# Kernel optimization log

Measured on AMD Instinct MI355X. Metric: run time of the kernel, lower is better.

Reference implementation:

```python
import jax, jax.numpy as jnp
import numpy as np

LAYERS = [2, 1024, 512, 256, 128, 1]
LB = jnp.array([0.0, 0.0], dtype=jnp.float32)
UB = jnp.array([2.0 * np.pi, 1.0], dtype=jnp.float32)


def _block_diag_mask(num_blocks, bs1, bs2):
    return jnp.kron(jnp.eye(num_blocks, dtype=jnp.float32), jnp.ones((bs1, bs2), jnp.float32))


def _masks():
    # masks for l in range(2, num_Layers - 2) with num_Layers = len(LAYERS) = 6 -> l in {2, 3}
    width = [LAYERS[0]] + [(2 ** (i - 1)) * LAYERS[i] for i in range(1, len(LAYERS) - 1)] + [LAYERS[-1]]
    masks = []
    for l in range(2, len(LAYERS) - 2):
        num_blocks = 2 ** (l - 1)
        bs1 = width[l] // num_blocks
        bs2 = 2 * LAYERS[l + 1]
        masks.append(_block_diag_mask(num_blocks, bs1, bs2))
    return masks


def setup_inputs() -> dict:
    key = jax.random.key(0)
    ks = jax.random.split(key, 8)
    N = 65536
    H = 1024

    def xavier(k, fi, fo):
        lim = float(np.sqrt(6.0 / (fi + fo)))
        return jax.random.uniform(k, (fi, fo), jnp.float32, -lim, lim)

    X = jax.random.uniform(ks[0], (N, 2), jnp.float32, 0.0, 1.0) * (UB - LB) + LB
    return {
        "X": X,
        "W0": xavier(ks[1], 2, H), "b0": jnp.zeros((1, H), jnp.float32),
        "W1": xavier(ks[2], H, H), "b1": jnp.zeros((1, H), jnp.float32),
        "W2": xavier(ks[3], H, H), "b2": jnp.zeros((1, H), jnp.float32),
        "W3": xavier(ks[4], H, H), "b3": jnp.zeros((1, H), jnp.float32),
        "W_last": xavier(ks[5], H, 1), "b_last": jnp.zeros((1, 1), jnp.float32),
    }


def reference(X, W0, b0, W1, b1, W2, b2, W3, b3, W_last, b_last):
    mask2, mask3 = _masks()
    # input normalization to [-1, 1]
    h = 2.0 * (X - LB) / (UB - LB) - 1.0
    h = jnp.tanh(h @ W0 + b0)                 # layer 0: dense
    h = jnp.tanh(h @ W1 + b1)                 # layer 1: dense (no mask in forward)
    h = jnp.tanh(h @ (W2 * mask2) + b2)       # layer 2: block-diagonal masked
    h = jnp.tanh(h @ (W3 * mask3) + b3)       # layer 3: block-diagonal masked
    return h @ W_last + b_last                # output layer, [N, 1]
```

## Files before the change

### kernel.cpp

```cpp
#include <hip/hip_runtime.h>
#include <cstdint>
#include <cstddef>


typedef _Float16  f16x8   __attribute__((ext_vector_type(8)));
typedef float     floatx4 __attribute__((ext_vector_type(4)));
typedef float     floatx8 __attribute__((ext_vector_type(8)));

__device__ __forceinline__ float tanh_fast(float x) {
    float e = __expf(2.0f * x);
    return 1.0f - 2.0f / (e + 1.0f);
}

__global__ __launch_bounds__(256)
void transposeH(const float* __restrict__ W, _Float16* __restrict__ Wt) {
    __shared__ float tile[32][33];
    const int tx = threadIdx.x & 31;
    const int ty = threadIdx.x >> 5;
    #pragma unroll
    for (int j = 0; j < 4; ++j) {
        int r = ty + j * 8;
        tile[r][tx] = W[(size_t)(blockIdx.y * 32 + r) * 1024 + blockIdx.x * 32 + tx];
    }
    __syncthreads();
    #pragma unroll
    for (int j = 0; j < 4; ++j) {
        int r = ty + j * 8;
        Wt[(size_t)(blockIdx.x * 32 + r) * 1024 + blockIdx.y * 32 + tx] =
            (_Float16)tile[tx][r];
    }
}

__global__ __launch_bounds__(256)
void init_out(float* __restrict__ out, const float* __restrict__ bl) {
    out[blockIdx.x * 256 + threadIdx.x] = bl[0];
}

__global__ __launch_bounds__(256)
void layer0_kernel(const float* __restrict__ X, const float* __restrict__ W0,
                   const float* __restrict__ b0, _Float16* __restrict__ H) {
    const int idx = blockIdx.x * 256 + threadIdx.x;
    const int row = idx >> 7;
    const int j0  = (idx & 127) << 3;
    const float x0 = X[row * 2 + 0];
    const float x1 = X[row * 2 + 1];
    const float xa = x0 * 0.31830988618379067f - 1.0f;
    const float xb = 2.0f * x1 - 1.0f;
    floatx8 wa = *(const floatx8*)(W0 + j0);
    floatx8 wb = *(const floatx8*)(W0 + 1024 + j0);
    floatx8 bb = *(const floatx8*)(b0 + j0);
    f16x8 o;
    #pragma unroll
    for (int j = 0; j < 8; ++j) {
        float v = fmaf(xa, wa[j], fmaf(xb, wb[j], bb[j]));
        o[j] = (_Float16)tanh_fast(v);
    }
    *(f16x8*)(H + (size_t)row * 1024 + j0) = o;
}

template <bool FUSE>
__global__ __launch_bounds__(512)
void gemm_tanh_f16(const _Float16* __restrict__ A, const _Float16* __restrict__ Bt,
                   const float* __restrict__ bias, _Float16* __restrict__ C,
                   const float* __restrict__ Wl, float* __restrict__ out, int KB) {
    __shared__ _Float16 As[256 * 32];
    __shared__ _Float16 Bs[128 * 32];

    const int tid  = threadIdx.x;
    const int lane = tid & 63;
    const int wave = tid >> 6;
    const int m0 = blockIdx.x * 256;
    const int n0 = blockIdx.y * 128;
    const int kbeg   = (n0 / KB) * KB;
    const int kiters = KB >> 5;
    const int wm = (wave & 3) << 6;
    const int wn = (wave >> 2) << 6;
    const int r = lane & 15;
    const int q = lane >> 4;

    const int rowA0 = tid >> 2;
    const int rowA1 = 128 + rowA0;
    const int seg   = (tid & 3) << 3;
    const size_t gA0 = (size_t)(m0 + rowA0) * 1024 + kbeg + seg;
    const size_t gA1 = (size_t)(m0 + rowA1) * 1024 + kbeg + seg;
    const size_t gB  = (size_t)(n0 + rowA0) * 1024 + kbeg + seg;
    const int ldsA0 = tid * 8;
    const int ldsA1 = (512 + tid) * 8;
    const int ldsB  = tid * 8;

    floatx4 acc[4][4];
    #pragma unroll
    for (int i = 0; i < 4; ++i)
        #pragma unroll
        for (int j = 0; j < 4; ++j)
            acc[i][j] = floatx4{0.f, 0.f, 0.f, 0.f};

    f16x8 va0 = *(const f16x8*)(A + gA0);
    f16x8 va1 = *(const f16x8*)(A + gA1);
    f16x8 vb  = *(const f16x8*)(Bt + gB);

    for (int t = 0; t < kiters; ++t) {
        __syncthreads();
        *(f16x8*)(As + ldsA0) = va0;
        *(f16x8*)(As + ldsA1) = va1;
        *(f16x8*)(Bs + ldsB)  = vb;
        __syncthreads();

        if (t + 1 < kiters) {
            const size_t d = (size_t)(t + 1) << 5;
            va0 = *(const f16x8*)(A + gA0 + d);
            va1 = *(const f16x8*)(A + gA1 + d);
            vb  = *(const f16x8*)(Bt + gB + d);
        }

        f16x8 af[4], bf[4];
        #pragma unroll
        for (int i = 0; i < 4; ++i) {
            af[i] = *(const f16x8*)(As + (wm + i * 16 + r) * 32 + q * 8);
            bf[i] = *(const f16x8*)(Bs + (wn + i * 16 + r) * 32 + q * 8);
        }
        #pragma unroll
        for (int i = 0; i < 4; ++i)
            #pragma unroll
            for (int j = 0; j < 4; ++j)
                acc[i][j] = __builtin_amdgcn_mfma_f32_16x16x32_f16(af[i], bf[j], acc[i][j], 0, 0, 0);
    }

    float bv[4], wlv[4];
    #pragma unroll
    for (int j = 0; j < 4; ++j) {
        const int col = n0 + wn + j * 16 + r;
        bv[j] = bias[col];
        if (FUSE) wlv[j] = Wl[col];
    }
    #pragma unroll
    for (int i = 0; i < 4; ++i) {
        const int row0 = m0 + wm + i * 16 + q * 4;
        #pragma unroll
        for (int rr = 0; rr < 4; ++rr) {
            if (!FUSE) {
                #pragma unroll
                for (int j = 0; j < 4; ++j) {
                    float o = tanh_fast(acc[i][j][rr] + bv[j]);
                    const int col = n0 + wn + j * 16 + r;
                    C[(size_t)(row0 + rr) * 1024 + col] = (_Float16)o;
                }
            } else {
                float p = 0.f;
                #pragma unroll
                for (int j = 0; j < 4; ++j)
                    p = fmaf(tanh_fast(acc[i][j][rr] + bv[j]), wlv[j], p);
                p += __shfl_down(p, 8);
                p += __shfl_down(p, 4);
                p += __shfl_down(p, 2);
                p += __shfl_down(p, 1);
                if (r == 0) atomicAdd(out + row0 + rr, p);
            }
        }
    }
}

extern "C" void kernel_launch(void* const* d_in, const int* in_sizes, int n_in,
                              void* d_out, int out_size, void* d_ws, size_t ws_size,
                              hipStream_t stream) {
    const float* X  = (const float*)d_in[0];
    const float* W0 = (const float*)d_in[1];
    const float* b0 = (const float*)d_in[2];
    const float* W1 = (const float*)d_in[3];
    const float* b1 = (const float*)d_in[4];
    const float* W2 = (const float*)d_in[5];
    const float* b2 = (const float*)d_in[6];
    const float* W3 = (const float*)d_in[7];
    const float* b3 = (const float*)d_in[8];
    const float* Wl = (const float*)d_in[9];
    const float* bl = (const float*)d_in[10];
    float* out = (float*)d_out;

    const int Nrows = in_sizes[0] / 2;
    const size_t WT = 1024 * 1024;
    const size_t wt_bytes = 3 * WT * 2;
    const size_t slack = 512;

    int R = 0;
    const int Rcap = Nrows < 32768 ? Nrows : 32768;
    for (int r = Rcap; r >= 256; r >>= 1)
        if ((size_t)2 * r * 2048 + wt_bytes + slack <= ws_size) { R = r; break; }
    if (!R) return;

    _Float16* wsp = (_Float16*)d_ws;
    _Float16* Wt1 = wsp;
    _Float16* Wt2 = Wt1 + WT;
    _Float16* Wt3 = Wt2 + WT;
    const size_t plane = (size_t)R * 1024;
    _Float16* P0 = Wt3 + WT;
    _Float16* P1 = P0 + plane;

    const dim3 tb(256);
    transposeH<<<dim3(32, 32), tb, 0, stream>>>(W1, Wt1);
    transposeH<<<dim3(32, 32), tb, 0, stream>>>(W2, Wt2);
    transposeH<<<dim3(32, 32), tb, 0, stream>>>(W3, Wt3);
    init_out<<<Nrows / 256, tb, 0, stream>>>(out, bl);

    const int nchunks = Nrows / R;
    for (int c = 0; c < nchunks; ++c) {
        const float* Xc = X + (size_t)c * R * 2;
        float* outc = out + (size_t)c * R;

        layer0_kernel<<<R / 2, tb, 0, stream>>>(Xc, W0, b0, P0);

        const dim3 tg(512);
        const dim3 gg(R / 256, 8);
        gemm_tanh_f16<false><<<gg, tg, 0, stream>>>(P0, Wt1, b1, P1, nullptr, nullptr, 1024);
        gemm_tanh_f16<false><<<gg, tg, 0, stream>>>(P1, Wt2, b2, P0, nullptr, nullptr, 512);
        gemm_tanh_f16<true ><<<gg, tg, 0, stream>>>(P0, Wt3, b3, nullptr, Wl, outc, 256);
    }
}
```

Baseline: 489.8 us.

## Rewrite GEMM with 256x256 tiles, direct-to-LDS loads and 4-stage pipeline

Replaces the register-staged, double-synced GEMM with a 256x256 tile kernel that issues global_load_lds transfers straight into a 4-deep LDS ring buffer, gated by vmcnt waits and a single barrier per k-step. LDS rows are XOR-swizzled to avoid bank conflicts, block IDs are remapped for L2 locality, and MFMA issue is wrapped in s_setprio. The larger per-wave tile (8x4 MFMA fragments) raises arithmetic intensity but doubles accumulator registers and uses 128KB of LDS, which limits occupancy. The epilogue loop is extended to cover the larger tile.

```diff
diff --git a/kernel.cpp b/kernel.cpp
--- a/kernel.cpp
+++ b/kernel.cpp
@@ -10,6 +10,12 @@
 __device__ __forceinline__ float tanh_fast(float x) {
     float e = __expf(2.0f * x);
     return 1.0f - 2.0f / (e + 1.0f);
+}
+
+__device__ __forceinline__ void gload16(const _Float16* g, _Float16* l) {
+    __builtin_amdgcn_global_load_lds(
+        (const __attribute__((address_space(1))) unsigned int*)g,
+        (__attribute__((address_space(3))) unsigned int*)l, 16, 0, 0);
 }
 
 __global__ __launch_bounds__(256)
@@ -59,72 +65,90 @@
 }
 
 template <bool FUSE>
-__global__ __launch_bounds__(512)
-void gemm_tanh_f16(const _Float16* __restrict__ A, const _Float16* __restrict__ Bt,
-                   const float* __restrict__ bias, _Float16* __restrict__ C,
-                   const float* __restrict__ Wl, float* __restrict__ out, int KB) {
-    __shared__ _Float16 As[256 * 32];
-    __shared__ _Float16 Bs[128 * 32];
+__global__ __launch_bounds__(512, 2)
+void gemm256(const _Float16* __restrict__ A, const _Float16* __restrict__ Bt,
+             const float* __restrict__ bias, _Float16* __restrict__ C,
+             const float* __restrict__ Wl, float* __restrict__ out, int KB) {
+    __shared__ _Float16 As[4 * 8192];
+    __shared__ _Float16 Bs[4 * 8192];
 
     const int tid  = threadIdx.x;
     const int lane = tid & 63;
-    const int wave = tid >> 6;
-    const int m0 = blockIdx.x * 256;
-    const int n0 = blockIdx.y * 128;
-    const int kbeg   = (n0 / KB) * KB;
-    const int kiters = KB >> 5;
-    const int wm = (wave & 3) << 6;
-    const int wn = (wave >> 2) << 6;
-    const int r = lane & 15;
-    const int q = lane >> 4;
-
-    const int rowA0 = tid >> 2;
-    const int rowA1 = 128 + rowA0;
-    const int seg   = (tid & 3) << 3;
-    const size_t gA0 = (size_t)(m0 + rowA0) * 1024 + kbeg + seg;
-    const size_t gA1 = (size_t)(m0 + rowA1) * 1024 + kbeg + seg;
-    const size_t gB  = (size_t)(n0 + rowA0) * 1024 + kbeg + seg;
-    const int ldsA0 = tid * 8;
-    const int ldsA1 = (512 + tid) * 8;
-    const int ldsB  = tid * 8;
-
-    floatx4 acc[4][4];
-    #pragma unroll
-    for (int i = 0; i < 4; ++i)
+    const int w    = tid >> 6;
+
+    const int total = gridDim.x * gridDim.y;
+    int lid = blockIdx.y * 4 + blockIdx.x;
+    if ((total & 7) == 0) {
+        const int qq = total >> 3;
+        lid = (lid & 7) * qq + (lid >> 3);
+    }
+    const int n0 = (lid & 3) << 8;
+    const int m0 = (lid >> 2) << 8;
+
+    const int kbeg = (n0 / KB) * KB;
+    const int NT   = KB >> 5;
+
+    const int c0  = w * 128 + lane;
+    const int c1  = c0 + 64;
+    const int rw0 = c0 >> 2, sl0 = (c0 & 3) ^ ((rw0 >> 1) & 3);
+    const int rw1 = c1 >> 2, sl1 = (c1 & 3) ^ ((rw1 >> 1) & 3);
+    const _Float16* gA0 = A  + (size_t)(m0 + rw0) * 1024 + kbeg + sl0 * 8;
+    const _Float16* gA1 = A  + (size_t)(m0 + rw1) * 1024 + kbeg + sl1 * 8;
+    const _Float16* gB0 = Bt + (size_t)(n0 + rw0) * 1024 + kbeg + sl0 * 8;
+    const _Float16* gB1 = Bt + (size_t)(n0 + rw1) * 1024 + kbeg + sl1 * 8;
+    const int ldsC0 = c0 * 8, ldsC1 = c1 * 8;
+
+    const int r   = lane & 15, q = lane >> 4;
+    const int swz = (q ^ ((r >> 1) & 3)) << 3;
+    const int wm  = (w & 1) << 7;
+    const int wn  = (w >> 1) << 6;
+
+    floatx4 acc[8][4];
+    #pragma unroll
+    for (int i = 0; i < 8; ++i)
         #pragma unroll
         for (int j = 0; j < 4; ++j)
             acc[i][j] = floatx4{0.f, 0.f, 0.f, 0.f};
 
-    f16x8 va0 = *(const f16x8*)(A + gA0);
-    f16x8 va1 = *(const f16x8*)(A + gA1);
-    f16x8 vb  = *(const f16x8*)(Bt + gB);
-
-    for (int t = 0; t < kiters; ++t) {
-        __syncthreads();
-        *(f16x8*)(As + ldsA0) = va0;
-        *(f16x8*)(As + ldsA1) = va1;
-        *(f16x8*)(Bs + ldsB)  = vb;
-        __syncthreads();
-
-        if (t + 1 < kiters) {
-            const size_t d = (size_t)(t + 1) << 5;
-            va0 = *(const f16x8*)(A + gA0 + d);
-            va1 = *(const f16x8*)(A + gA1 + d);
-            vb  = *(const f16x8*)(Bt + gB + d);
-        }
-
-        f16x8 af[4], bf[4];
-        #pragma unroll
-        for (int i = 0; i < 4; ++i) {
-            af[i] = *(const f16x8*)(As + (wm + i * 16 + r) * 32 + q * 8);
-            bf[i] = *(const f16x8*)(Bs + (wn + i * 16 + r) * 32 + q * 8);
-        }
-        #pragma unroll
-        for (int i = 0; i < 4; ++i)
+#define STAGE(tt) do {                                        \
+        const int _s  = ((tt) & 3) * 8192;                    \
+        const int _ko = (tt) * 32;                            \
+        gload16(gA0 + _ko, As + _s + ldsC0);                  \
+        gload16(gA1 + _ko, As + _s + ldsC1);                  \
+        gload16(gB0 + _ko, Bs + _s + ldsC0);                  \
+        gload16(gB1 + _ko, Bs + _s + ldsC1);                  \
+    } while (0)
+
+    STAGE(0); STAGE(1); STAGE(2);
+
+    for (int t = 0; t < NT; ++t) {
+        if (t < NT - 2)       asm volatile("s_waitcnt vmcnt(8)" ::: "memory");
+        else if (t == NT - 2) asm volatile("s_waitcnt vmcnt(4)" ::: "memory");
+        else                  asm volatile("s_waitcnt vmcnt(0)" ::: "memory");
+        __builtin_amdgcn_s_barrier();
+        asm volatile("" ::: "memory");
+
+        if (t + 3 < NT) STAGE(t + 3);
+
+        const _Float16* At = As + (t & 3) * 8192;
+        const _Float16* Bw = Bs + (t & 3) * 8192;
+        f16x8 af[8], bf[4];
+        #pragma unroll
+        for (int i = 0; i < 8; ++i)
+            af[i] = *(const f16x8*)(At + (wm + i * 16 + r) * 32 + swz);
+        #pragma unroll
+        for (int j = 0; j < 4; ++j)
+            bf[j] = *(const f16x8*)(Bw + (wn + j * 16 + r) * 32 + swz);
+
+        __builtin_amdgcn_s_setprio(1);
+        #pragma unroll
+        for (int i = 0; i < 8; ++i)
             #pragma unroll
             for (int j = 0; j < 4; ++j)
                 acc[i][j] = __builtin_amdgcn_mfma_f32_16x16x32_f16(af[i], bf[j], acc[i][j], 0, 0, 0);
-    }
+        __builtin_amdgcn_s_setprio(0);
+    }
+#undef STAGE
 
     float bv[4], wlv[4];
     #pragma unroll
@@ -134,7 +158,7 @@
         if (FUSE) wlv[j] = Wl[col];
     }
     #pragma unroll
-    for (int i = 0; i < 4; ++i) {
+    for (int i = 0; i < 8; ++i) {
         const int row0 = m0 + wm + i * 16 + q * 4;
         #pragma unroll
         for (int rr = 0; rr < 4; ++rr) {
@@ -209,9 +233,9 @@
         layer0_kernel<<<R / 2, tb, 0, stream>>>(Xc, W0, b0, P0);
 
         const dim3 tg(512);
-        const dim3 gg(R / 256, 8);
-        gemm_tanh_f16<false><<<gg, tg, 0, stream>>>(P0, Wt1, b1, P1, nullptr, nullptr, 1024);
-        gemm_tanh_f16<false><<<gg, tg, 0, stream>>>(P1, Wt2, b2, P0, nullptr, nullptr, 512);
-        gemm_tanh_f16<true ><<<gg, tg, 0, stream>>>(P0, Wt3, b3, nullptr, Wl, outc, 256);
-    }
-}
+        const dim3 gg(4, R / 256);
+        gemm256<false><<<gg, tg, 0, stream>>>(P0, Wt1, b1, P1, nullptr, nullptr, 1024);
+        gemm256<false><<<gg, tg, 0, stream>>>(P1, Wt2, b2, P0, nullptr, nullptr, 512);
+        gemm256<true ><<<gg, tg, 0, stream>>>(P0, Wt3, b3, nullptr, Wl, outc, 256);
+    }
+}
```

Measured after the change: 548.2 us. 1.12x slower.

## Fuse whole MLP forward into one kernel keeping activations in LDS

Applied to the files above, without the earlier changes.

Replaces the per-layer kernels with a single fused kernel where each 512-thread block owns 64 rows and keeps the full 64x1024 fp16 activation tile in 128KB of shared memory across all layers. Weights are streamed straight from global memory into registers per wave, double-buffered across k-steps, and activations use an XOR swizzle to avoid bank conflicts. The final dot product with the output weights is reduced in shared memory, so the atomics and the init kernel are gone. This removes the global round trips for intermediate activations and the extra launches, but each block re-reads the weights from L2 with no LDS reuse, and occupancy is limited to one block per CU.

```diff
diff --git a/kernel.cpp b/kernel.cpp
--- a/kernel.cpp
+++ b/kernel.cpp
@@ -31,132 +31,169 @@
     }
 }
 
-__global__ __launch_bounds__(256)
-void init_out(float* __restrict__ out, const float* __restrict__ bl) {
-    out[blockIdx.x * 256 + threadIdx.x] = bl[0];
-}
-
-__global__ __launch_bounds__(256)
-void layer0_kernel(const float* __restrict__ X, const float* __restrict__ W0,
-                   const float* __restrict__ b0, _Float16* __restrict__ H) {
-    const int idx = blockIdx.x * 256 + threadIdx.x;
-    const int row = idx >> 7;
-    const int j0  = (idx & 127) << 3;
-    const float x0 = X[row * 2 + 0];
-    const float x1 = X[row * 2 + 1];
-    const float xa = x0 * 0.31830988618379067f - 1.0f;
-    const float xb = 2.0f * x1 - 1.0f;
-    floatx8 wa = *(const floatx8*)(W0 + j0);
-    floatx8 wb = *(const floatx8*)(W0 + 1024 + j0);
-    floatx8 bb = *(const floatx8*)(b0 + j0);
-    f16x8 o;
+template <int KSTEPS>
+__device__ __forceinline__ void gemm_layer(const _Float16* __restrict__ Wt,
+                                           const _Float16* h, int kbeg,
+                                           int wn, int r, int q,
+                                           floatx4 (&acc)[4][8]) {
+    const int swzm = (r & 7) << 3;
+    const _Float16* wb = Wt + (size_t)(wn + r) * 1024 + kbeg + q * 8;
+    const _Float16* hb = h + r * 1024;
+
+    f16x8 bfA[8], bfB[8];
+    #pragma unroll
+    for (int j = 0; j < 8; ++j)
+        bfA[j] = *(const f16x8*)(wb + j * 16384);
+
+    #pragma unroll
+    for (int tt = 0; tt < KSTEPS / 2; ++tt) {
+        const int k0 = kbeg + tt * 64;
+        #pragma unroll
+        for (int j = 0; j < 8; ++j)
+            bfB[j] = *(const f16x8*)(wb + j * 16384 + tt * 64 + 32);
+
+        f16x8 af[4];
+        #pragma unroll
+        for (int i = 0; i < 4; ++i)
+            af[i] = *(const f16x8*)(hb + i * 16384 + ((k0 + q * 8) ^ swzm));
+        #pragma unroll
+        for (int i = 0; i < 4; ++i)
+            #pragma unroll
+            for (int j = 0; j < 8; ++j)
+                acc[i][j] = __builtin_amdgcn_mfma_f32_16x16x32_f16(af[i], bfA[j], acc[i][j], 0, 0, 0);
+
+        if (tt + 1 < KSTEPS / 2) {
+            #pragma unroll
+            for (int j = 0; j < 8; ++j)
+                bfA[j] = *(const f16x8*)(wb + j * 16384 + tt * 64 + 64);
+        }
+
+        #pragma unroll
+        for (int i = 0; i < 4; ++i)
+            af[i] = *(const f16x8*)(hb + i * 16384 + ((k0 + 32 + q * 8) ^ swzm));
+        #pragma unroll
+        for (int i = 0; i < 4; ++i)
+            #pragma unroll
+            for (int j = 0; j < 8; ++j)
+                acc[i][j] = __builtin_amdgcn_mfma_f32_16x16x32_f16(af[i], bfB[j], acc[i][j], 0, 0, 0);
+    }
+}
+
+__device__ __forceinline__ void store_h(_Float16* h, const float* __restrict__ bias,
+                                        const floatx4 (&acc)[4][8],
+                                        int wn, int r, int q) {
     #pragma unroll
     for (int j = 0; j < 8; ++j) {
-        float v = fmaf(xa, wa[j], fmaf(xb, wb[j], bb[j]));
-        o[j] = (_Float16)tanh_fast(v);
-    }
-    *(f16x8*)(H + (size_t)row * 1024 + j0) = o;
-}
-
-template <bool FUSE>
+        const int col = wn + j * 16 + r;
+        const float bv = bias[col];
+        #pragma unroll
+        for (int i = 0; i < 4; ++i) {
+            #pragma unroll
+            for (int rr = 0; rr < 4; ++rr) {
+                const int row = i * 16 + q * 4 + rr;
+                h[row * 1024 + (col ^ ((row & 7) << 3))] =
+                    (_Float16)tanh_fast(acc[i][j][rr] + bv);
+            }
+        }
+    }
+}
+
 __global__ __launch_bounds__(512)
-void gemm_tanh_f16(const _Float16* __restrict__ A, const _Float16* __restrict__ Bt,
-                   const float* __restrict__ bias, _Float16* __restrict__ C,
-                   const float* __restrict__ Wl, float* __restrict__ out, int KB) {
-    __shared__ _Float16 As[256 * 32];
-    __shared__ _Float16 Bs[128 * 32];
+void fused_forward(const float* __restrict__ X, const float* __restrict__ W0,
+                   const float* __restrict__ b0,
+                   const _Float16* __restrict__ Wt1, const float* __restrict__ b1,
+                   const _Float16* __restrict__ Wt2, const float* __restrict__ b2,
+                   const _Float16* __restrict__ Wt3, const float* __restrict__ b3,
+                   const float* __restrict__ Wl, const float* __restrict__ bl,
+                   float* __restrict__ out) {
+    __shared__ _Float16 h[64 * 1024];
 
     const int tid  = threadIdx.x;
     const int lane = tid & 63;
-    const int wave = tid >> 6;
-    const int m0 = blockIdx.x * 256;
-    const int n0 = blockIdx.y * 128;
-    const int kbeg   = (n0 / KB) * KB;
-    const int kiters = KB >> 5;
-    const int wm = (wave & 3) << 6;
-    const int wn = (wave >> 2) << 6;
-    const int r = lane & 15;
-    const int q = lane >> 4;
-
-    const int rowA0 = tid >> 2;
-    const int rowA1 = 128 + rowA0;
-    const int seg   = (tid & 3) << 3;
-    const size_t gA0 = (size_t)(m0 + rowA0) * 1024 + kbeg + seg;
-    const size_t gA1 = (size_t)(m0 + rowA1) * 1024 + kbeg + seg;
-    const size_t gB  = (size_t)(n0 + rowA0) * 1024 + kbeg + seg;
-    const int ldsA0 = tid * 8;
-    const int ldsA1 = (512 + tid) * 8;
-    const int ldsB  = tid * 8;
-
-    floatx4 acc[4][4];
+    const int w    = tid >> 6;
+    const int r    = lane & 15, q = lane >> 4;
+    const int wn   = w << 7;
+    const int row0 = blockIdx.x << 6;
+
+    {
+        const int frow  = tid >> 3;
+        const int fcol0 = (tid & 7) << 7;
+        const float x0 = X[(row0 + frow) * 2 + 0];
+        const float x1 = X[(row0 + frow) * 2 + 1];
+        const float xa = x0 * 0.31830988618379067f - 1.0f;
+        const float xb = 2.0f * x1 - 1.0f;
+        const int fswz = (frow & 7) << 3;
+        #pragma unroll
+        for (int c = 0; c < 128; c += 8) {
+            const int col = fcol0 + c;
+            floatx8 wa = *(const floatx8*)(W0 + col);
+            floatx8 wv = *(const floatx8*)(W0 + 1024 + col);
+            floatx8 bb = *(const floatx8*)(b0 + col);
+            f16x8 o;
+            #pragma unroll
+            for (int jj = 0; jj < 8; ++jj)
+                o[jj] = (_Float16)tanh_fast(fmaf(xa, wa[jj], fmaf(xb, wv[jj], bb[jj])));
+            *(f16x8*)(h + frow * 1024 + (col ^ fswz)) = o;
+        }
+    }
+    __syncthreads();
+
+    floatx4 acc[4][8];
+
     #pragma unroll
     for (int i = 0; i < 4; ++i)
         #pragma unroll
-        for (int j = 0; j < 4; ++j)
-            acc[i][j] = floatx4{0.f, 0.f, 0.f, 0.f};
-
-    f16x8 va0 = *(const f16x8*)(A + gA0);
-    f16x8 va1 = *(const f16x8*)(A + gA1);
-    f16x8 vb  = *(const f16x8*)(Bt + gB);
-
-    for (int t = 0; t < kiters; ++t) {
-        __syncthreads();
-        *(f16x8*)(As + ldsA0) = va0;
-        *(f16x8*)(As + ldsA1) = va1;
-        *(f16x8*)(Bs + ldsB)  = vb;
-        __syncthreads();
-
-        if (t + 1 < kiters) {
-            const size_t d = (size_t)(t + 1) << 5;
-            va0 = *(const f16x8*)(A + gA0 + d);
-            va1 = *(const f16x8*)(A + gA1 + d);
-            vb  = *(const f16x8*)(Bt + gB + d);
-        }
-
-        f16x8 af[4], bf[4];
-        #pragma unroll
-        for (int i = 0; i < 4; ++i) {
-            af[i] = *(const f16x8*)(As + (wm + i * 16 + r) * 32 + q * 8);
-            bf[i] = *(const f16x8*)(Bs + (wn + i * 16 + r) * 32 + q * 8);
-        }
-        #pragma unroll
-        for (int i = 0; i < 4; ++i)
-            #pragma unroll
-            for (int j = 0; j < 4; ++j)
-                acc[i][j] = __builtin_amdgcn_mfma_f32_16x16x32_f16(af[i], bf[j], acc[i][j], 0, 0, 0);
-    }
-
-    float bv[4], wlv[4];
-    #pragma unroll
-    for (int j = 0; j < 4; ++j) {
-        const int col = n0 + wn + j * 16 + r;
-        bv[j] = bias[col];
-        if (FUSE) wlv[j] = Wl[col];
-    }
+        for (int j = 0; j < 8; ++j) acc[i][j] = floatx4{0.f, 0.f, 0.f, 0.f};
+    gemm_layer<32>(Wt1, h, 0, wn, r, q, acc);
+    __syncthreads();
+    store_h(h, b1, acc, wn, r, q);
+    __syncthreads();
+
+    #pragma unroll
+    for (int i = 0; i < 4; ++i)
+        #pragma unroll
+        for (int j = 0; j < 8; ++j) acc[i][j] = floatx4{0.f, 0.f, 0.f, 0.f};
+    gemm_layer<16>(Wt2, h, (wn >> 9) << 9, wn, r, q, acc);
+    __syncthreads();
+    store_h(h, b2, acc, wn, r, q);
+    __syncthreads();
+
+    #pragma unroll
+    for (int i = 0; i < 4; ++i)
+        #pragma unroll
+        for (int j = 0; j < 8; ++j) acc[i][j] = floatx4{0.f, 0.f, 0.f, 0.f};
+    gemm_layer<8>(Wt3, h, (wn >> 8) << 8, wn, r, q, acc);
+
+    float bv[8], wl[8];
+    #pragma unroll
+    for (int j = 0; j < 8; ++j) {
+        const int col = wn + j * 16 + r;
+        bv[j] = b3[col];
+        wl[j] = Wl[col];
+    }
+    __syncthreads();
+    float* red = (float*)h;
     #pragma unroll
     for (int i = 0; i < 4; ++i) {
-        const int row0 = m0 + wm + i * 16 + q * 4;
         #pragma unroll
         for (int rr = 0; rr < 4; ++rr) {
-            if (!FUSE) {
-                #pragma unroll
-                for (int j = 0; j < 4; ++j) {
-                    float o = tanh_fast(acc[i][j][rr] + bv[j]);
-                    const int col = n0 + wn + j * 16 + r;
-                    C[(size_t)(row0 + rr) * 1024 + col] = (_Float16)o;
-                }
-            } else {
-                float p = 0.f;
-                #pragma unroll
-                for (int j = 0; j < 4; ++j)
-                    p = fmaf(tanh_fast(acc[i][j][rr] + bv[j]), wlv[j], p);
-                p += __shfl_down(p, 8);
-                p += __shfl_down(p, 4);
-                p += __shfl_down(p, 2);
-                p += __shfl_down(p, 1);
-                if (r == 0) atomicAdd(out + row0 + rr, p);
-            }
-        }
+            float p = 0.f;
+            #pragma unroll
+            for (int j = 0; j < 8; ++j)
+                p = fmaf(tanh_fast(acc[i][j][rr] + bv[j]), wl[j], p);
+            p += __shfl_down(p, 8);
+            p += __shfl_down(p, 4);
+            p += __shfl_down(p, 2);
+            p += __shfl_down(p, 1);
+            if (r == 0) red[w * 64 + i * 16 + q * 4 + rr] = p;
+        }
+    }
+    __syncthreads();
+    if (tid < 64) {
+        float s = bl[0];
+        #pragma unroll
+        for (int ww = 0; ww < 8; ++ww) s += red[ww * 64 + tid];
+        out[row0 + tid] = s;
     }
 }
 
@@ -178,40 +215,17 @@
 
     const int Nrows = in_sizes[0] / 2;
     const size_t WT = 1024 * 1024;
-    const size_t wt_bytes = 3 * WT * 2;
-    const size_t slack = 512;
-
-    int R = 0;
-    const int Rcap = Nrows < 32768 ? Nrows : 32768;
-    for (int r = Rcap; r >= 256; r >>= 1)
-        if ((size_t)2 * r * 2048 + wt_bytes + slack <= ws_size) { R = r; break; }
-    if (!R) return;
-
-    _Float16* wsp = (_Float16*)d_ws;
-    _Float16* Wt1 = wsp;
+
+    if (ws_size < 3 * WT * 2) return;
+    _Float16* Wt1 = (_Float16*)d_ws;
     _Float16* Wt2 = Wt1 + WT;
     _Float16* Wt3 = Wt2 + WT;
-    const size_t plane = (size_t)R * 1024;
-    _Float16* P0 = Wt3 + WT;
-    _Float16* P1 = P0 + plane;
 
     const dim3 tb(256);
     transposeH<<<dim3(32, 32), tb, 0, stream>>>(W1, Wt1);
     transposeH<<<dim3(32, 32), tb, 0, stream>>>(W2, Wt2);
     transposeH<<<dim3(32, 32), tb, 0, stream>>>(W3, Wt3);
-    init_out<<<Nrows / 256, tb, 0, stream>>>(out, bl);
-
-    const int nchunks = Nrows / R;
-    for (int c = 0; c < nchunks; ++c) {
-        const float* Xc = X + (size_t)c * R * 2;
-        float* outc = out + (size_t)c * R;
-
-        layer0_kernel<<<R / 2, tb, 0, stream>>>(Xc, W0, b0, P0);
-
-        const dim3 tg(512);
-        const dim3 gg(R / 256, 8);
-        gemm_tanh_f16<false><<<gg, tg, 0, stream>>>(P0, Wt1, b1, P1, nullptr, nullptr, 1024);
-        gemm_tanh_f16<false><<<gg, tg, 0, stream>>>(P1, Wt2, b2, P0, nullptr, nullptr, 512);
-        gemm_tanh_f16<true ><<<gg, tg, 0, stream>>>(P0, Wt3, b3, nullptr, Wl, outc, 256);
-    }
-}
+
+    fused_forward<<<dim3(Nrows / 64), dim3(512), 0, stream>>>(
+        X, W0, b0, Wt1, b1, Wt2, b2, Wt3, b3, Wl, bl, out);
+}
```

Result: slower. 727.0 us (+48.4%).
